# Kernel optimization log

Hardware: AMD Instinct MI355X
Metric: run time of the kernel (lower is better)

## Reference

```python
import jax, jax.numpy as jnp
import numpy as np

NBINS = 128


def setup_inputs() -> dict:
    key = jax.random.key(0)
    feats = jax.random.normal(key, (100000, 8), dtype=jnp.float32)
    return {"feats": feats}


def reference(feats):
    # feats: [N, V]. setup=True path: fmin/fmax computed from feats itself.
    nvars = feats.shape[1]
    fmin = feats.min(axis=0)  # [V]
    fmax = feats.max(axis=0)  # [V]
    # torch.linspace(min, max, nbins) per variable -> [V, NBINS]
    t = jnp.arange(NBINS, dtype=feats.dtype) / (NBINS - 1)
    lin = fmin[:, None] + (fmax - fmin)[:, None] * t[None, :]
    step = lin[:, 1] - lin[:, 0]  # [V]
    # dense diff matrix, rounded to 6 decimals (np.around = round-half-even)
    diff = jnp.round((lin[None, :, :] - feats[:, :, None]) * 1e6) / 1e6  # [N, V, NBINS]
    # torch: cur_diff[cur_diff > 0] = cur_diff.min()  (min over that var's whole [N, NBINS] slab)
    mn = diff.min(axis=(0, 2), keepdims=True)  # [1, V, 1]
    masked = jnp.where(diff > 0, mn, diff)
    bins = jnp.argmax(masked, axis=2)  # [N, V], first max like torch
    # value of the chosen bin edge per sample/var
    vals = lin[jnp.arange(nvars)[None, :], bins]  # [N, V]
    regs = jnp.clip(feats - vals, 0.0, None) / step[None, :]
    return bins, regs
```

## Files before the change

kernel.cpp:

```cpp
#include <hip/hip_runtime.h>
#include <math.h>

#define NV 8
#define NBINS 128
#define GRID_A 64


__global__ __launch_bounds__(256) void k_colminmax(const float* __restrict__ feats,
                                                   float* __restrict__ ws, int n) {
    const int tid = threadIdx.x;
    const int gt = blockIdx.x * blockDim.x + tid;
    const int nth = blockDim.x * gridDim.x;
    float lmin[NV], lmax[NV];
#pragma unroll
    for (int c = 0; c < NV; ++c) { lmin[c] = __builtin_inff(); lmax[c] = -__builtin_inff(); }
    const int n4 = n >> 2;
    const float4* f4 = (const float4*)feats;
    if (((gt << 2) & 7) == 0) {
        for (int q = gt; q < n4; q += nth) {
            float4 v = f4[q];
            lmin[0] = fminf(lmin[0], v.x); lmax[0] = fmaxf(lmax[0], v.x);
            lmin[1] = fminf(lmin[1], v.y); lmax[1] = fmaxf(lmax[1], v.y);
            lmin[2] = fminf(lmin[2], v.z); lmax[2] = fmaxf(lmax[2], v.z);
            lmin[3] = fminf(lmin[3], v.w); lmax[3] = fmaxf(lmax[3], v.w);
        }
    } else {
        for (int q = gt; q < n4; q += nth) {
            float4 v = f4[q];
            lmin[4] = fminf(lmin[4], v.x); lmax[4] = fmaxf(lmax[4], v.x);
            lmin[5] = fminf(lmin[5], v.y); lmax[5] = fmaxf(lmax[5], v.y);
            lmin[6] = fminf(lmin[6], v.z); lmax[6] = fmaxf(lmax[6], v.z);
            lmin[7] = fminf(lmin[7], v.w); lmax[7] = fmaxf(lmax[7], v.w);
        }
    }
    for (int i = (n4 << 2) + gt; i < n; i += nth) {
        float v = feats[i];
        int c = i & 7;
#pragma unroll
        for (int cc = 0; cc < NV; ++cc)
            if (cc == c) { lmin[cc] = fminf(lmin[cc], v); lmax[cc] = fmaxf(lmax[cc], v); }
    }
#pragma unroll
    for (int c = 0; c < NV; ++c) {
        float mn = lmin[c], mx = lmax[c];
#pragma unroll
        for (int m = 32; m >= 1; m >>= 1) {
            mn = fminf(mn, __shfl_xor(mn, m));
            mx = fmaxf(mx, __shfl_xor(mx, m));
        }
        lmin[c] = mn; lmax[c] = mx;
    }
    __shared__ float smin[4][NV], smax[4][NV];
    const int wave = tid >> 6, lane = tid & 63;
    if (lane == 0) {
#pragma unroll
        for (int c = 0; c < NV; ++c) { smin[wave][c] = lmin[c]; smax[wave][c] = lmax[c]; }
    }
    __syncthreads();
    if (tid < NV) {
        float mn = fminf(fminf(smin[0][tid], smin[1][tid]), fminf(smin[2][tid], smin[3][tid]));
        float mx = fmaxf(fmaxf(smax[0][tid], smax[1][tid]), fmaxf(smax[2][tid], smax[3][tid]));
        ws[blockIdx.x * NV + tid] = mn;
        ws[GRID_A * NV + blockIdx.x * NV + tid] = mx;
    }
}

__global__ __launch_bounds__(64) void k_combine(float* __restrict__ ws) {
    const int t = threadIdx.x;
    float mn[NV], mx[NV];
#pragma unroll
    for (int c = 0; c < NV; ++c) {
        mn[c] = ws[t * NV + c];
        mx[c] = ws[GRID_A * NV + t * NV + c];
    }
#pragma unroll
    for (int c = 0; c < NV; ++c) {
#pragma unroll
        for (int m = 32; m >= 1; m >>= 1) {
            mn[c] = fminf(mn[c], __shfl_xor(mn[c], m));
            mx[c] = fmaxf(mx[c], __shfl_xor(mx[c], m));
        }
    }
    if (t == 0) {
#pragma unroll
        for (int c = 0; c < NV; ++c) {
            ws[2 * GRID_A * NV + c] = mn[c];
            ws[2 * GRID_A * NV + NV + c] = mx[c];
        }
    }
}

__global__ __launch_bounds__(256) void k_quantize(const float* __restrict__ feats,
                                                  const float* __restrict__ ws,
                                                  float* __restrict__ out, int n) {
    __shared__ float slin[NV * 129];
    __shared__ float sfmin[NV], sstep[NV];
    const int tid = threadIdx.x;
    const float* fm = ws + 2 * GRID_A * NV;
    for (int e = tid; e < NV * NBINS; e += blockDim.x) {
        int v = e >> 7;
        int b = e & 127;
        float fmin = fm[v];
        float range = __fsub_rn(fm[NV + v], fmin);
        float tb = __fdiv_rn((float)b, 127.0f);
        slin[v * 129 + b] = __fadd_rn(fmin, __fmul_rn(range, tb));
    }
    __syncthreads();
    if (tid < NV) {
        sfmin[tid] = slin[tid * 129 + 0];
        sstep[tid] = __fsub_rn(slin[tid * 129 + 1], slin[tid * 129 + 0]);
    }
    __syncthreads();
    const int i = blockIdx.x * blockDim.x + tid;
    if (i >= n) return;
    const int v = i & 7;
    const float feat = feats[i];
    const float fmin = sfmin[v];
    const float step = sstep[v];
    const float* lv = &slin[v * 129];
    int b = (int)floorf((feat - fmin) / step);
    b = b < 0 ? 0 : (b > 127 ? 127 : b);
    while (b < NBINS - 1 &&
           rintf(__fmul_rn(__fsub_rn(lv[b + 1], feat), 1.0e6f)) <= 0.0f) ++b;
    while (b > 0 &&
           rintf(__fmul_rn(__fsub_rn(lv[b], feat), 1.0e6f)) > 0.0f) --b;
    const float val = lv[b];
    const float reg = __fdiv_rn(fmaxf(__fsub_rn(feat, val), 0.0f), step);
    out[i] = (float)b;
    out[n + i] = reg;
}

extern "C" void kernel_launch(void* const* d_in, const int* in_sizes, int n_in,
                              void* d_out, int out_size, void* d_ws, size_t ws_size,
                              hipStream_t stream) {
    const float* feats = (const float*)d_in[0];
    float* ws = (float*)d_ws;
    float* out = (float*)d_out;
    const int n = in_sizes[0];
    k_colminmax<<<GRID_A, 256, 0, stream>>>(feats, ws, n);
    k_combine<<<1, 64, 0, stream>>>(ws);
    k_quantize<<<(n + 255) / 256, 256, 0, stream>>>(feats, ws, out, n);
}
```

Measured before the change: 69.70 us.

## Fuse min/max reduction and quantization into one cooperative kernel with grid sync

Replaces the three launches (partial column min/max, combine, quantize) with a single cooperative kernel. A grid-wide sync separates the partial reduction from the final reduction, which every block now repeats redundantly. The quantize phase uses a grid-stride float4 loop so each thread handles four features and writes vectorized outputs. This is meant to remove launch overhead and inter-kernel gaps, at the cost of cooperative-launch and grid-sync overhead and a fixed grid of 256 blocks.

```diff
diff --git a/kernel.cpp b/kernel.cpp
--- a/kernel.cpp
+++ b/kernel.cpp
@@ -1,22 +1,49 @@
 #include <hip/hip_runtime.h>
+#include <hip/hip_cooperative_groups.h>
 #include <math.h>
+
+namespace cg = cooperative_groups;
 
 #define NV 8
 #define NBINS 128
-#define GRID_A 64
+#define GRID 256
+#define TPB 256
 
 
-__global__ __launch_bounds__(256) void k_colminmax(const float* __restrict__ feats,
-                                                   float* __restrict__ ws, int n) {
+__device__ __forceinline__ void quant_one(float feat, const float* __restrict__ lv,
+                                          float fmin, float step,
+                                          float& bin_out, float& reg_out) {
+    int b = (int)floorf((feat - fmin) / step);
+    b = b < 0 ? 0 : (b > NBINS - 1 ? NBINS - 1 : b);
+    while (b < NBINS - 1 &&
+           rintf(__fmul_rn(__fsub_rn(lv[b + 1], feat), 1.0e6f)) <= 0.0f) ++b;
+    while (b > 0 &&
+           rintf(__fmul_rn(__fsub_rn(lv[b], feat), 1.0e6f)) > 0.0f) --b;
+    const float val = lv[b];
+    bin_out = (float)b;
+    reg_out = __fdiv_rn(fmaxf(__fsub_rn(feat, val), 0.0f), step);
+}
+
+__global__ __launch_bounds__(TPB) void k_fused(const float* __restrict__ feats,
+                                               float* __restrict__ ws,
+                                               float* __restrict__ out, int n) {
     const int tid = threadIdx.x;
-    const int gt = blockIdx.x * blockDim.x + tid;
-    const int nth = blockDim.x * gridDim.x;
+    const int bid = blockIdx.x;
+    const int gt = bid * TPB + tid;
+    const int nth = GRID * TPB;
+    const int wave = tid >> 6, lane = tid & 63;
+
+    __shared__ float swmin[4][NV], swmax[4][NV];
+    __shared__ float sfmin[NV], sfmax[NV], sstep[NV];
+    __shared__ float slin[NV * 129];
+
     float lmin[NV], lmax[NV];
 #pragma unroll
     for (int c = 0; c < NV; ++c) { lmin[c] = __builtin_inff(); lmax[c] = -__builtin_inff(); }
+
     const int n4 = n >> 2;
     const float4* f4 = (const float4*)feats;
-    if (((gt << 2) & 7) == 0) {
+    if ((gt & 1) == 0) {
         for (int q = gt; q < n4; q += nth) {
             float4 v = f4[q];
             lmin[0] = fminf(lmin[0], v.x); lmax[0] = fmaxf(lmax[0], v.x);
@@ -42,92 +69,100 @@
     }
 #pragma unroll
     for (int c = 0; c < NV; ++c) {
-        float mn = lmin[c], mx = lmax[c];
 #pragma unroll
         for (int m = 32; m >= 1; m >>= 1) {
-            mn = fminf(mn, __shfl_xor(mn, m));
-            mx = fmaxf(mx, __shfl_xor(mx, m));
+            lmin[c] = fminf(lmin[c], __shfl_xor(lmin[c], m));
+            lmax[c] = fmaxf(lmax[c], __shfl_xor(lmax[c], m));
         }
-        lmin[c] = mn; lmax[c] = mx;
     }
-    __shared__ float smin[4][NV], smax[4][NV];
-    const int wave = tid >> 6, lane = tid & 63;
     if (lane == 0) {
 #pragma unroll
-        for (int c = 0; c < NV; ++c) { smin[wave][c] = lmin[c]; smax[wave][c] = lmax[c]; }
+        for (int c = 0; c < NV; ++c) { swmin[wave][c] = lmin[c]; swmax[wave][c] = lmax[c]; }
     }
     __syncthreads();
     if (tid < NV) {
-        float mn = fminf(fminf(smin[0][tid], smin[1][tid]), fminf(smin[2][tid], smin[3][tid]));
-        float mx = fmaxf(fmaxf(smax[0][tid], smax[1][tid]), fmaxf(smax[2][tid], smax[3][tid]));
-        ws[blockIdx.x * NV + tid] = mn;
-        ws[GRID_A * NV + blockIdx.x * NV + tid] = mx;
+        float mn = fminf(fminf(swmin[0][tid], swmin[1][tid]), fminf(swmin[2][tid], swmin[3][tid]));
+        float mx = fmaxf(fmaxf(swmax[0][tid], swmax[1][tid]), fmaxf(swmax[2][tid], swmax[3][tid]));
+        ws[bid * NV + tid] = mn;
+        ws[GRID * NV + bid * NV + tid] = mx;
     }
-}
 
-__global__ __launch_bounds__(64) void k_combine(float* __restrict__ ws) {
-    const int t = threadIdx.x;
-    float mn[NV], mx[NV];
-#pragma unroll
-    for (int c = 0; c < NV; ++c) {
-        mn[c] = ws[t * NV + c];
-        mx[c] = ws[GRID_A * NV + t * NV + c];
-    }
-#pragma unroll
-    for (int c = 0; c < NV; ++c) {
-#pragma unroll
-        for (int m = 32; m >= 1; m >>= 1) {
-            mn[c] = fminf(mn[c], __shfl_xor(mn[c], m));
-            mx[c] = fmaxf(mx[c], __shfl_xor(mx[c], m));
-        }
-    }
-    if (t == 0) {
+    cg::this_grid().sync();
+
+    {
+        const float4* p4 = (const float4*)ws;
+        float4 a = p4[2 * tid], b = p4[2 * tid + 1];
+        float4 c4 = p4[2 * GRID + 2 * tid], d = p4[2 * GRID + 2 * tid + 1];
+        float mn[NV] = {a.x, a.y, a.z, a.w, b.x, b.y, b.z, b.w};
+        float mx[NV] = {c4.x, c4.y, c4.z, c4.w, d.x, d.y, d.z, d.w};
 #pragma unroll
         for (int c = 0; c < NV; ++c) {
-            ws[2 * GRID_A * NV + c] = mn[c];
-            ws[2 * GRID_A * NV + NV + c] = mx[c];
+#pragma unroll
+            for (int m = 32; m >= 1; m >>= 1) {
+                mn[c] = fminf(mn[c], __shfl_xor(mn[c], m));
+                mx[c] = fmaxf(mx[c], __shfl_xor(mx[c], m));
+            }
         }
+        __syncthreads();
+        if (lane == 0) {
+#pragma unroll
+            for (int c = 0; c < NV; ++c) { swmin[wave][c] = mn[c]; swmax[wave][c] = mx[c]; }
+        }
+        __syncthreads();
+        if (tid < NV) {
+            sfmin[tid] = fminf(fminf(swmin[0][tid], swmin[1][tid]), fminf(swmin[2][tid], swmin[3][tid]));
+            sfmax[tid] = fmaxf(fmaxf(swmax[0][tid], swmax[1][tid]), fmaxf(swmax[2][tid], swmax[3][tid]));
+        }
+        __syncthreads();
     }
-}
 
-__global__ __launch_bounds__(256) void k_quantize(const float* __restrict__ feats,
-                                                  const float* __restrict__ ws,
-                                                  float* __restrict__ out, int n) {
-    __shared__ float slin[NV * 129];
-    __shared__ float sfmin[NV], sstep[NV];
-    const int tid = threadIdx.x;
-    const float* fm = ws + 2 * GRID_A * NV;
-    for (int e = tid; e < NV * NBINS; e += blockDim.x) {
+    for (int e = tid; e < NV * NBINS; e += TPB) {
         int v = e >> 7;
         int b = e & 127;
-        float fmin = fm[v];
-        float range = __fsub_rn(fm[NV + v], fmin);
+        float fmin = sfmin[v];
+        float range = __fsub_rn(sfmax[v], fmin);
         float tb = __fdiv_rn((float)b, 127.0f);
         slin[v * 129 + b] = __fadd_rn(fmin, __fmul_rn(range, tb));
     }
     __syncthreads();
-    if (tid < NV) {
-        sfmin[tid] = slin[tid * 129 + 0];
+    if (tid < NV)
         sstep[tid] = __fsub_rn(slin[tid * 129 + 1], slin[tid * 129 + 0]);
+    __syncthreads();
+
+    float4* outb = (float4*)out;
+    float* outr_base = out + n;
+    if ((n & 3) == 0) {
+        float4* outr = (float4*)outr_base;
+        if ((gt & 1) == 0) {
+            for (int q = gt; q < n4; q += nth) {
+                float4 v = f4[q];
+                float4 bb, rr;
+                quant_one(v.x, &slin[0 * 129], sfmin[0], sstep[0], bb.x, rr.x);
+                quant_one(v.y, &slin[1 * 129], sfmin[1], sstep[1], bb.y, rr.y);
+                quant_one(v.z, &slin[2 * 129], sfmin[2], sstep[2], bb.z, rr.z);
+                quant_one(v.w, &slin[3 * 129], sfmin[3], sstep[3], bb.w, rr.w);
+                outb[q] = bb; outr[q] = rr;
+            }
+        } else {
+            for (int q = gt; q < n4; q += nth) {
+                float4 v = f4[q];
+                float4 bb, rr;
+                quant_one(v.x, &slin[4 * 129], sfmin[4], sstep[4], bb.x, rr.x);
+                quant_one(v.y, &slin[5 * 129], sfmin[5], sstep[5], bb.y, rr.y);
+                quant_one(v.z, &slin[6 * 129], sfmin[6], sstep[6], bb.z, rr.z);
+                quant_one(v.w, &slin[7 * 129], sfmin[7], sstep[7], bb.w, rr.w);
+                outb[q] = bb; outr[q] = rr;
+            }
+        }
+    } else {
+        for (int i = gt; i < n; i += nth) {
+            int v = i & 7;
+            float bb, rr;
+            quant_one(feats[i], &slin[v * 129], sfmin[v], sstep[v], bb, rr);
+            out[i] = bb; outr_base[i] = rr;
+        }
     }
-    __syncthreads();
-    const int i = blockIdx.x * blockDim.x + tid;
-    if (i >= n) return;
-    const int v = i & 7;
-    const float feat = feats[i];
-    const float fmin = sfmin[v];
-    const float step = sstep[v];
-    const float* lv = &slin[v * 129];
-    int b = (int)floorf((feat - fmin) / step);
-    b = b < 0 ? 0 : (b > 127 ? 127 : b);
-    while (b < NBINS - 1 &&
-           rintf(__fmul_rn(__fsub_rn(lv[b + 1], feat), 1.0e6f)) <= 0.0f) ++b;
-    while (b > 0 &&
-           rintf(__fmul_rn(__fsub_rn(lv[b], feat), 1.0e6f)) > 0.0f) --b;
-    const float val = lv[b];
-    const float reg = __fdiv_rn(fmaxf(__fsub_rn(feat, val), 0.0f), step);
-    out[i] = (float)b;
-    out[n + i] = reg;
+    if ((n & 3) == 0) return;
 }
 
 extern "C" void kernel_launch(void* const* d_in, const int* in_sizes, int n_in,
@@ -136,8 +171,7 @@
     const float* feats = (const float*)d_in[0];
     float* ws = (float*)d_ws;
     float* out = (float*)d_out;
-    const int n = in_sizes[0];
-    k_colminmax<<<GRID_A, 256, 0, stream>>>(feats, ws, n);
-    k_combine<<<1, 64, 0, stream>>>(ws);
-    k_quantize<<<(n + 255) / 256, 256, 0, stream>>>(feats, ws, out, n);
+    int n = in_sizes[0];
+    void* args[] = { (void*)&feats, (void*)&ws, (void*)&out, (void*)&n };
+    hipLaunchCooperativeKernel((const void*)k_fused, dim3(GRID), dim3(TPB), args, 0, stream);
 }
```

Result: slower. 103.6 us (+48.6%).
